# Performance work log

Measured on AMD Instinct MI355X. Metric: run time of the kernel, lower is better.

Reference implementation:

```python
import jax, jax.numpy as jnp
import numpy as np

TOP_K = 2


def setup_inputs() -> dict:
    key = jax.random.key(0)
    ks = jax.random.split(key, 6)
    B, S, H, F, E = 4, 2048, 1024, 4096, 8
    x = jax.random.normal(ks[0], (B, S, H), dtype=jnp.float32)
    gate_w = jax.random.normal(ks[1], (E, H), dtype=jnp.float32) * 0.02
    W1 = jax.random.normal(ks[2], (E, H, F), dtype=jnp.float32) * (1.0 / np.sqrt(H))
    b1 = jnp.zeros((E, F), dtype=jnp.float32)
    W2 = jax.random.normal(ks[3], (E, F, H), dtype=jnp.float32) * (1.0 / np.sqrt(F))
    b2 = jnp.zeros((E, H), dtype=jnp.float32)
    sW1 = jax.random.normal(ks[4], (H, F), dtype=jnp.float32) * (1.0 / np.sqrt(H))
    sb1 = jnp.zeros((F,), dtype=jnp.float32)
    sW2 = jax.random.normal(ks[5], (F, H), dtype=jnp.float32) * (1.0 / np.sqrt(F))
    sb2 = jnp.zeros((H,), dtype=jnp.float32)
    return {"x": x, "gate_w": gate_w, "W1": W1, "b1": b1, "W2": W2, "b2": b2,
            "sW1": sW1, "sb1": sb1, "sW2": sW2, "sb2": sb2}


def reference(x, gate_w, W1, b1, W2, b2, sW1, sb1, sW2, sb2):
    B, S, H = x.shape
    E = gate_w.shape[0]
    x_flat = x.reshape(-1, H)                                  # [T, H]
    # --- router ---
    logits = x_flat @ gate_w.T                                 # [T, E]
    probs = jax.nn.softmax(logits.astype(jnp.float32), axis=-1)
    top_w, sel = jax.lax.top_k(probs, TOP_K)                   # [T, K], [T, K]
    top_w = top_w / jnp.sum(top_w, axis=-1, keepdims=True)
    # combine weights: zero for unselected experts -> faithful to masked gather/scatter
    combine = jnp.sum(jax.nn.one_hot(sel, E, dtype=top_w.dtype) * top_w[..., None], axis=1)  # [T, E]
    combine = combine.astype(x.dtype)
    # --- experts (dense grouped GEMM; unselected tokens contribute with weight 0) ---
    h = jax.nn.gelu(jnp.einsum('th,ehf->tef', x_flat, W1) + b1[None], approximate=False)
    y = jnp.einsum('tef,efh->teh', h, W2) + b2[None]           # [T, E, H]
    out = jnp.einsum('teh,te->th', y, combine)                 # [T, H]
    # --- shared expert ---
    sh = jax.nn.gelu(x_flat @ sW1 + sb1, approximate=False)
    out = out + sh @ sW2 + sb2
    return out.reshape(B, S, H)
```

## Files before the change

kernel.cpp:

```cpp
#include <hip/hip_runtime.h>
#include <hip/hip_bf16.h>

#define T_TOKENS 8192
#define H_DIM 1024
#define F_DIM 4096
#define N_EXP 8
#define MAX_SLOTS 25600
#define MAX_TILES 200

typedef __attribute__((ext_vector_type(8))) short short8;
typedef __attribute__((ext_vector_type(4))) float floatx4;

__device__ __forceinline__ float gelu_f(float v) {
    return 0.5f * v * (1.0f + erff(v * 0.70710678118654752440f));
}

__device__ __forceinline__ void gload_lds16(const void* g, void* l) {
    __builtin_amdgcn_global_load_lds((const __attribute__((address_space(1))) void*)g,
                                     (__attribute__((address_space(3))) void*)l,
                                     16, 0, 0);
}

__global__ __launch_bounds__(256) void convert_x_kernel(const float* __restrict__ x,
                                                        unsigned long long* __restrict__ xb,
                                                        int n4) {
    int i = blockIdx.x * 256 + threadIdx.x;
    if (i >= n4) return;
    floatx4 v = ((const floatx4*)x)[i];
    union { __hip_bfloat16 h[4]; unsigned long long u; } p;
    p.h[0] = __float2bfloat16(v.x);
    p.h[1] = __float2bfloat16(v.y);
    p.h[2] = __float2bfloat16(v.z);
    p.h[3] = __float2bfloat16(v.w);
    xb[i] = p.u;
}

__global__ __launch_bounds__(256) void transpose_convert_kernel(const float* __restrict__ in,
                                                                __hip_bfloat16* __restrict__ out,
                                                                int R, int C) {
    const float* inm = in + (size_t)blockIdx.z * R * C;
    __hip_bfloat16* outm = out + (size_t)blockIdx.z * R * C;
    __shared__ float tile[32][33];
    int r0 = blockIdx.x * 32;
    int c0 = blockIdx.y * 32;
    int tx = threadIdx.x & 31, ty = threadIdx.x >> 5;
#pragma unroll
    for (int i = 0; i < 4; i++)
        tile[ty + 8 * i][tx] = inm[(size_t)(r0 + ty + 8 * i) * C + c0 + tx];
    __syncthreads();
#pragma unroll
    for (int i = 0; i < 4; i++)
        outm[(size_t)(c0 + ty + 8 * i) * R + r0 + tx] = __float2bfloat16(tile[tx][ty + 8 * i]);
}

__global__ __launch_bounds__(256) void router_kernel(const float* __restrict__ x,
                                                     const float* __restrict__ gw,
                                                     int* __restrict__ sel_e,
                                                     float* __restrict__ sel_w,
                                                     int* __restrict__ counts) {
    int wave = threadIdx.x >> 6, lane = threadIdx.x & 63;
    int t = blockIdx.x * 4 + wave;
    const float* xt = x + (size_t)t * H_DIM;
    float acc[N_EXP];
#pragma unroll
    for (int e = 0; e < N_EXP; e++) acc[e] = 0.f;
    for (int i = 0; i < H_DIM; i += 64) {
        float xv = xt[i + lane];
#pragma unroll
        for (int e = 0; e < N_EXP; e++) acc[e] += xv * gw[e * H_DIM + i + lane];
    }
#pragma unroll
    for (int e = 0; e < N_EXP; e++) {
#pragma unroll
        for (int off = 32; off > 0; off >>= 1) acc[e] += __shfl_down(acc[e], off);
    }
    if (lane == 0) {
        float m = acc[0];
#pragma unroll
        for (int e = 1; e < N_EXP; e++) m = fmaxf(m, acc[e]);
        float p[N_EXP];
#pragma unroll
        for (int e = 0; e < N_EXP; e++) p[e] = expf(acc[e] - m);
        int i1 = 0;
#pragma unroll
        for (int e = 1; e < N_EXP; e++) if (p[e] > p[i1]) i1 = e;
        int i2 = (i1 == 0) ? 1 : 0;
#pragma unroll
        for (int e = 0; e < N_EXP; e++) if (e != i1 && p[e] > p[i2]) i2 = e;
        float s = p[i1] + p[i2];
        sel_e[2 * t]     = i1;
        sel_e[2 * t + 1] = i2;
        sel_w[2 * t]     = p[i1] / s;
        sel_w[2 * t + 1] = p[i2] / s;
        atomicAdd(&counts[i1], 1);
        atomicAdd(&counts[i2], 1);
    }
}

__global__ void offsets_kernel(const int* __restrict__ counts, int* __restrict__ off) {
    if (threadIdx.x == 0 && blockIdx.x == 0) {
        int o = 0;
#pragma unroll
        for (int e = 0; e < N_EXP; e++) {
            off[e] = o;
            o += ((counts[e] + 127) >> 7) << 7;
        }
        off[8] = o;
        off[9] = o + T_TOKENS;
    }
}

__global__ __launch_bounds__(256) void scatter_kernel(const int* __restrict__ sel_e,
                                                      const float* __restrict__ sel_w,
                                                      const int* __restrict__ off,
                                                      int* __restrict__ pos,
                                                      int* __restrict__ slot_token,
                                                      float* __restrict__ slot_weight) {
    int t = blockIdx.x * 256 + threadIdx.x;
    if (t >= T_TOKENS) return;
#pragma unroll
    for (int k = 0; k < 2; k++) {
        int e = sel_e[2 * t + k];
        int p = atomicAdd(&pos[e], 1);
        int s = off[e] + p;
        slot_token[s] = t;
        slot_weight[s] = sel_w[2 * t + k];
    }
    int s = off[8] + t;
    slot_token[s] = t;
    slot_weight[s] = 1.0f;
}

__global__ __launch_bounds__(256) void gemm1_kernel(const __hip_bfloat16* __restrict__ xb,
                                                    const __hip_bfloat16* __restrict__ w1t,
                                                    const __hip_bfloat16* __restrict__ sw1t,
                                                    const float* __restrict__ b1,
                                                    const float* __restrict__ sb1,
                                                    const int* __restrict__ slot_token,
                                                    const int* __restrict__ off,
                                                    __hip_bfloat16* __restrict__ h_buf) {
    int row0 = blockIdx.x * 128;
    if (row0 >= off[9]) return;
    int f0 = blockIdx.y * 128;
    int e = 8;
#pragma unroll
    for (int i = 0; i < 8; i++)
        if (row0 >= off[i] && row0 < off[i + 1]) e = i;
    const __hip_bfloat16* Bp = (e < 8) ? (w1t + (size_t)e * F_DIM * H_DIM) : sw1t;
    const float* bias = (e < 8) ? (b1 + (size_t)e * F_DIM) : sb1;

    __shared__ __align__(16) __hip_bfloat16 As[128 * 32];
    __shared__ __align__(16) __hip_bfloat16 Bs[128 * 32];

    int tid = threadIdx.x;
    int rA = tid >> 2, cc = tid & 3;
    int tok0 = slot_token[row0 + rA];
    int tok1 = slot_token[row0 + 64 + rA];
    int t0c = tok0 >= 0 ? tok0 : 0;
    int t1c = tok1 >= 0 ? tok1 : 0;
    const __hip_bfloat16* a0 = xb + (size_t)t0c * H_DIM + cc * 8;
    const __hip_bfloat16* a1 = xb + (size_t)t1c * H_DIM + cc * 8;
    const __hip_bfloat16* b0 = Bp + (size_t)(f0 + rA) * H_DIM + cc * 8;
    const __hip_bfloat16* b1r = Bp + (size_t)(f0 + 64 + rA) * H_DIM + cc * 8;

    int lane = tid & 63, wid = tid >> 6;
    char* asb0 = (char*)As + wid * 1024;
    char* asb1 = (char*)As + 4096 + wid * 1024;
    char* bsb0 = (char*)Bs + wid * 1024;
    char* bsb1 = (char*)Bs + 4096 + wid * 1024;

    int wm = (wid >> 1) * 64, wn = (wid & 1) * 64;
    int lr = lane & 15, q = lane >> 4;

    floatx4 acc[4][4] = {};

    for (int k0 = 0; k0 < H_DIM; k0 += 32) {
        gload_lds16(a0 + k0, asb0);
        gload_lds16(a1 + k0, asb1);
        gload_lds16(b0 + k0, bsb0);
        gload_lds16(b1r + k0, bsb1);
        __syncthreads();
        short8 af[4], bfr[4];
#pragma unroll
        for (int mt = 0; mt < 4; mt++) af[mt] = *(const short8*)(&As[(wm + mt * 16 + lr) * 32 + q * 8]);
#pragma unroll
        for (int nt = 0; nt < 4; nt++) bfr[nt] = *(const short8*)(&Bs[(wn + nt * 16 + lr) * 32 + q * 8]);
#pragma unroll
        for (int mt = 0; mt < 4; mt++)
#pragma unroll
            for (int nt = 0; nt < 4; nt++)
                acc[mt][nt] = __builtin_amdgcn_mfma_f32_16x16x32_bf16(af[mt], bfr[nt], acc[mt][nt], 0, 0, 0);
        __syncthreads();
    }

#pragma unroll
    for (int mt = 0; mt < 4; mt++) {
#pragma unroll
        for (int r = 0; r < 4; r++) {
            int row = wm + mt * 16 + q * 4 + r;
            int slot = row0 + row;
            int tok = slot_token[slot];
            __hip_bfloat16* hp = h_buf + (size_t)slot * F_DIM + f0;
#pragma unroll
            for (int nt = 0; nt < 4; nt++) {
                int col = wn + nt * 16 + lr;
                float v = acc[mt][nt][r] + bias[f0 + col];
                hp[col] = __float2bfloat16(tok >= 0 ? gelu_f(v) : 0.0f);
            }
        }
    }
}

__global__ __launch_bounds__(256) void gemm2_kernel(const __hip_bfloat16* __restrict__ h_buf,
                                                    const __hip_bfloat16* __restrict__ w2t,
                                                    const __hip_bfloat16* __restrict__ sw2t,
                                                    const float* __restrict__ b2,
                                                    const float* __restrict__ sb2,
                                                    const int* __restrict__ slot_token,
                                                    const float* __restrict__ slot_weight,
                                                    const int* __restrict__ off,
                                                    float* __restrict__ out) {
    int row0 = blockIdx.y * 128;
    if (row0 >= off[9]) return;
    int h0 = blockIdx.x * 128;
    int e = 8;
#pragma unroll
    for (int i = 0; i < 8; i++)
        if (row0 >= off[i] && row0 < off[i + 1]) e = i;
    const __hip_bfloat16* Bp = (e < 8) ? (w2t + (size_t)e * H_DIM * F_DIM) : sw2t;
    const float* bias = (e < 8) ? (b2 + (size_t)e * H_DIM) : sb2;

    __shared__ __align__(16) __hip_bfloat16 As[128 * 32];
    __shared__ __align__(16) __hip_bfloat16 Bs[128 * 32];

    int tid = threadIdx.x;
    int rA = tid >> 2, cc = tid & 3;
    const __hip_bfloat16* a0 = h_buf + (size_t)(row0 + rA) * F_DIM + cc * 8;
    const __hip_bfloat16* a1 = h_buf + (size_t)(row0 + 64 + rA) * F_DIM + cc * 8;
    const __hip_bfloat16* b0 = Bp + (size_t)(h0 + rA) * F_DIM + cc * 8;
    const __hip_bfloat16* b1r = Bp + (size_t)(h0 + 64 + rA) * F_DIM + cc * 8;

    int lane = tid & 63, wid = tid >> 6;
    char* asb0 = (char*)As + wid * 1024;
    char* asb1 = (char*)As + 4096 + wid * 1024;
    char* bsb0 = (char*)Bs + wid * 1024;
    char* bsb1 = (char*)Bs + 4096 + wid * 1024;

    int wm = (wid >> 1) * 64, wn = (wid & 1) * 64;
    int lr = lane & 15, q = lane >> 4;

    floatx4 acc[4][4] = {};

    for (int k0 = 0; k0 < F_DIM; k0 += 32) {
        gload_lds16(a0 + k0, asb0);
        gload_lds16(a1 + k0, asb1);
        gload_lds16(b0 + k0, bsb0);
        gload_lds16(b1r + k0, bsb1);
        __syncthreads();
        short8 af[4], bfr[4];
#pragma unroll
        for (int mt = 0; mt < 4; mt++) af[mt] = *(const short8*)(&As[(wm + mt * 16 + lr) * 32 + q * 8]);
#pragma unroll
        for (int nt = 0; nt < 4; nt++) bfr[nt] = *(const short8*)(&Bs[(wn + nt * 16 + lr) * 32 + q * 8]);
#pragma unroll
        for (int mt = 0; mt < 4; mt++)
#pragma unroll
            for (int nt = 0; nt < 4; nt++)
                acc[mt][nt] = __builtin_amdgcn_mfma_f32_16x16x32_bf16(af[mt], bfr[nt], acc[mt][nt], 0, 0, 0);
        __syncthreads();
    }

#pragma unroll
    for (int mt = 0; mt < 4; mt++) {
#pragma unroll
        for (int r = 0; r < 4; r++) {
            int row = wm + mt * 16 + q * 4 + r;
            int slot = row0 + row;
            int tok = slot_token[slot];
            if (tok >= 0) {
                float w = slot_weight[slot];
                float* op = out + (size_t)tok * H_DIM + h0;
#pragma unroll
                for (int nt = 0; nt < 4; nt++) {
                    int col = wn + nt * 16 + lr;
                    atomicAdd(&op[col], w * (acc[mt][nt][r] + bias[h0 + col]));
                }
            }
        }
    }
}

extern "C" void kernel_launch(void* const* d_in, const int* in_sizes, int n_in,
                              void* d_out, int out_size, void* d_ws, size_t ws_size,
                              hipStream_t stream) {
    (void)in_sizes; (void)n_in; (void)ws_size;
    const float* x   = (const float*)d_in[0];
    const float* gw  = (const float*)d_in[1];
    const float* W1  = (const float*)d_in[2];
    const float* b1  = (const float*)d_in[3];
    const float* W2  = (const float*)d_in[4];
    const float* b2  = (const float*)d_in[5];
    const float* sW1 = (const float*)d_in[6];
    const float* sb1 = (const float*)d_in[7];
    const float* sW2 = (const float*)d_in[8];
    const float* sb2 = (const float*)d_in[9];
    float* out = (float*)d_out;

    char* ws = (char*)d_ws;
    size_t o = 0;
    auto alloc = [&](size_t bytes) -> void* {
        void* p = ws + o;
        o += (bytes + 255) & ~(size_t)255;
        return p;
    };
    __hip_bfloat16* xb    = (__hip_bfloat16*)alloc((size_t)T_TOKENS * H_DIM * 2);
    __hip_bfloat16* w1t   = (__hip_bfloat16*)alloc((size_t)N_EXP * H_DIM * F_DIM * 2);
    __hip_bfloat16* w2t   = (__hip_bfloat16*)alloc((size_t)N_EXP * H_DIM * F_DIM * 2);
    __hip_bfloat16* sw1t  = (__hip_bfloat16*)alloc((size_t)H_DIM * F_DIM * 2);
    __hip_bfloat16* sw2t  = (__hip_bfloat16*)alloc((size_t)H_DIM * F_DIM * 2);
    __hip_bfloat16* h_buf = (__hip_bfloat16*)alloc((size_t)MAX_SLOTS * F_DIM * 2);
    int*   slot_token  = (int*)alloc(MAX_SLOTS * 4);
    float* slot_weight = (float*)alloc(MAX_SLOTS * 4);
    int*   sel_e = (int*)alloc((size_t)T_TOKENS * 2 * 4);
    float* sel_w = (float*)alloc((size_t)T_TOKENS * 2 * 4);
    int*   ctrl  = (int*)alloc(64 * 4);
    int* counts = ctrl;
    int* pos    = ctrl + 8;
    int* off    = ctrl + 16;

    hipMemsetAsync(d_out, 0, (size_t)out_size * sizeof(float), stream);
    hipMemsetAsync(ctrl, 0, 64 * 4, stream);
    hipMemsetAsync(slot_token, 0xFF, MAX_SLOTS * 4, stream);

    int n4 = T_TOKENS * H_DIM / 4;
    convert_x_kernel<<<(n4 + 255) / 256, 256, 0, stream>>>(x, (unsigned long long*)xb, n4);

    transpose_convert_kernel<<<dim3(H_DIM / 32, F_DIM / 32, N_EXP), 256, 0, stream>>>(W1, w1t, H_DIM, F_DIM);
    transpose_convert_kernel<<<dim3(F_DIM / 32, H_DIM / 32, N_EXP), 256, 0, stream>>>(W2, w2t, F_DIM, H_DIM);
    transpose_convert_kernel<<<dim3(H_DIM / 32, F_DIM / 32, 1), 256, 0, stream>>>(sW1, sw1t, H_DIM, F_DIM);
    transpose_convert_kernel<<<dim3(F_DIM / 32, H_DIM / 32, 1), 256, 0, stream>>>(sW2, sw2t, F_DIM, H_DIM);

    router_kernel<<<T_TOKENS / 4, 256, 0, stream>>>(x, gw, sel_e, sel_w, counts);
    offsets_kernel<<<1, 64, 0, stream>>>(counts, off);
    scatter_kernel<<<T_TOKENS / 256, 256, 0, stream>>>(sel_e, sel_w, off, pos, slot_token, slot_weight);

    gemm1_kernel<<<dim3(MAX_TILES, F_DIM / 128), 256, 0, stream>>>(
        xb, w1t, sw1t, b1, sb1, slot_token, off, h_buf);
    gemm2_kernel<<<dim3(H_DIM / 128, MAX_TILES), 256, 0, stream>>>(
        h_buf, w2t, sw2t, b2, sb2, slot_token, slot_weight, off, out);
}
```

Baseline: 1.558 ms.

## Double-buffer GEMM LDS tiles, vectorize weight transpose, reorder gemm1 grid

```diff
diff --git a/kernel.cpp b/kernel.cpp
--- a/kernel.cpp
+++ b/kernel.cpp
@@ -40,17 +40,30 @@
                                                                 int R, int C) {
     const float* inm = in + (size_t)blockIdx.z * R * C;
     __hip_bfloat16* outm = out + (size_t)blockIdx.z * R * C;
-    __shared__ float tile[32][33];
-    int r0 = blockIdx.x * 32;
-    int c0 = blockIdx.y * 32;
-    int tx = threadIdx.x & 31, ty = threadIdx.x >> 5;
-#pragma unroll
-    for (int i = 0; i < 4; i++)
-        tile[ty + 8 * i][tx] = inm[(size_t)(r0 + ty + 8 * i) * C + c0 + tx];
+    __shared__ float tile[64][65];
+    int r0 = blockIdx.x * 64, c0 = blockIdx.y * 64;
+    int t = threadIdx.x;
+    int cr = t & 15;
+    int rr = t >> 4;
+#pragma unroll
+    for (int i = 0; i < 4; i++) {
+        floatx4 v = *(const floatx4*)(inm + (size_t)(r0 + rr + 16 * i) * C + c0 + cr * 4);
+        tile[rr + 16 * i][cr * 4 + 0] = v.x;
+        tile[rr + 16 * i][cr * 4 + 1] = v.y;
+        tile[rr + 16 * i][cr * 4 + 2] = v.z;
+        tile[rr + 16 * i][cr * 4 + 3] = v.w;
+    }
     __syncthreads();
-#pragma unroll
-    for (int i = 0; i < 4; i++)
-        outm[(size_t)(c0 + ty + 8 * i) * R + r0 + tx] = __float2bfloat16(tile[tx][ty + 8 * i]);
+    int cw = t >> 3;
+    int rw = (t & 7) * 8;
+#pragma unroll
+    for (int i = 0; i < 2; i++) {
+        int c = cw + 32 * i;
+        union { __hip_bfloat16 h[8]; short8 s; } p;
+#pragma unroll
+        for (int j = 0; j < 8; j++) p.h[j] = __float2bfloat16(tile[rw + j][c]);
+        *(short8*)(outm + (size_t)(c0 + c) * R + r0 + rw) = p.s;
+    }
 }
 
 __global__ __launch_bounds__(256) void router_kernel(const float* __restrict__ x,
@@ -139,9 +152,9 @@
                                                     const int* __restrict__ slot_token,
                                                     const int* __restrict__ off,
                                                     __hip_bfloat16* __restrict__ h_buf) {
-    int row0 = blockIdx.x * 128;
+    int row0 = blockIdx.y * 128;
     if (row0 >= off[9]) return;
-    int f0 = blockIdx.y * 128;
+    int f0 = blockIdx.x * 128;
     int e = 8;
 #pragma unroll
     for (int i = 0; i < 8; i++)
@@ -149,8 +162,8 @@
     const __hip_bfloat16* Bp = (e < 8) ? (w1t + (size_t)e * F_DIM * H_DIM) : sw1t;
     const float* bias = (e < 8) ? (b1 + (size_t)e * F_DIM) : sb1;
 
-    __shared__ __align__(16) __hip_bfloat16 As[128 * 32];
-    __shared__ __align__(16) __hip_bfloat16 Bs[128 * 32];
+    __shared__ __align__(16) __hip_bfloat16 As[2 * 128 * 32];
+    __shared__ __align__(16) __hip_bfloat16 Bs[2 * 128 * 32];
 
     int tid = threadIdx.x;
     int rA = tid >> 2, cc = tid & 3;
@@ -164,33 +177,42 @@
     const __hip_bfloat16* b1r = Bp + (size_t)(f0 + 64 + rA) * H_DIM + cc * 8;
 
     int lane = tid & 63, wid = tid >> 6;
-    char* asb0 = (char*)As + wid * 1024;
-    char* asb1 = (char*)As + 4096 + wid * 1024;
-    char* bsb0 = (char*)Bs + wid * 1024;
-    char* bsb1 = (char*)Bs + 4096 + wid * 1024;
+    char* asb = (char*)As + wid * 1024;
+    char* bsb = (char*)Bs + wid * 1024;
 
     int wm = (wid >> 1) * 64, wn = (wid & 1) * 64;
     int lr = lane & 15, q = lane >> 4;
 
     floatx4 acc[4][4] = {};
 
-    for (int k0 = 0; k0 < H_DIM; k0 += 32) {
-        gload_lds16(a0 + k0, asb0);
-        gload_lds16(a1 + k0, asb1);
-        gload_lds16(b0 + k0, bsb0);
-        gload_lds16(b1r + k0, bsb1);
+    gload_lds16(a0, asb);
+    gload_lds16(a1, asb + 4096);
+    gload_lds16(b0, bsb);
+    gload_lds16(b1r, bsb + 4096);
+
+    int buf = 0;
+    for (int k0 = 0; k0 < H_DIM; k0 += 32, buf ^= 1) {
         __syncthreads();
+        if (k0 + 32 < H_DIM) {
+            int kn = k0 + 32;
+            int bo = (buf ^ 1) * 8192;
+            gload_lds16(a0 + kn, asb + bo);
+            gload_lds16(a1 + kn, asb + bo + 4096);
+            gload_lds16(b0 + kn, bsb + bo);
+            gload_lds16(b1r + kn, bsb + bo + 4096);
+        }
+        const __hip_bfloat16* Ab = As + buf * 4096;
+        const __hip_bfloat16* Bb = Bs + buf * 4096;
         short8 af[4], bfr[4];
 #pragma unroll
-        for (int mt = 0; mt < 4; mt++) af[mt] = *(const short8*)(&As[(wm + mt * 16 + lr) * 32 + q * 8]);
-#pragma unroll
-        for (int nt = 0; nt < 4; nt++) bfr[nt] = *(const short8*)(&Bs[(wn + nt * 16 + lr) * 32 + q * 8]);
+        for (int mt = 0; mt < 4; mt++) af[mt] = *(const short8*)(&Ab[(wm + mt * 16 + lr) * 32 + q * 8]);
+#pragma unroll
+        for (int nt = 0; nt < 4; nt++) bfr[nt] = *(const short8*)(&Bb[(wn + nt * 16 + lr) * 32 + q * 8]);
 #pragma unroll
         for (int mt = 0; mt < 4; mt++)
 #pragma unroll
             for (int nt = 0; nt < 4; nt++)
                 acc[mt][nt] = __builtin_amdgcn_mfma_f32_16x16x32_bf16(af[mt], bfr[nt], acc[mt][nt], 0, 0, 0);
-        __syncthreads();
     }
 
 #pragma unroll
@@ -230,8 +252,8 @@
     const __hip_bfloat16* Bp = (e < 8) ? (w2t + (size_t)e * H_DIM * F_DIM) : sw2t;
     const float* bias = (e < 8) ? (b2 + (size_t)e * H_DIM) : sb2;
 
-    __shared__ __align__(16) __hip_bfloat16 As[128 * 32];
-    __shared__ __align__(16) __hip_bfloat16 Bs[128 * 32];
+    __shared__ __align__(16) __hip_bfloat16 As[2 * 128 * 32];
+    __shared__ __align__(16) __hip_bfloat16 Bs[2 * 128 * 32];
 
     int tid = threadIdx.x;
     int rA = tid >> 2, cc = tid & 3;
@@ -241,33 +263,42 @@
     const __hip_bfloat16* b1r = Bp + (size_t)(h0 + 64 + rA) * F_DIM + cc * 8;
 
     int lane = tid & 63, wid = tid >> 6;
-    char* asb0 = (char*)As + wid * 1024;
-    char* asb1 = (char*)As + 4096 + wid * 1024;
-    char* bsb0 = (char*)Bs + wid * 1024;
-    char* bsb1 = (char*)Bs + 4096 + wid * 1024;
+    char* asb = (char*)As + wid * 1024;
+    char* bsb = (char*)Bs + wid * 1024;
 
     int wm = (wid >> 1) * 64, wn = (wid & 1) * 64;
     int lr = lane & 15, q = lane >> 4;
 
     floatx4 acc[4][4] = {};
 
-    for (int k0 = 0; k0 < F_DIM; k0 += 32) {
-        gload_lds16(a0 + k0, asb0);
-        gload_lds16(a1 + k0, asb1);
-        gload_lds16(b0 + k0, bsb0);
-        gload_lds16(b1r + k0, bsb1);
+    gload_lds16(a0, asb);
+    gload_lds16(a1, asb + 4096);
+    gload_lds16(b0, bsb);
+    gload_lds16(b1r, bsb + 4096);
+
+    int buf = 0;
+    for (int k0 = 0; k0 < F_DIM; k0 += 32, buf ^= 1) {
         __syncthreads();
+        if (k0 + 32 < F_DIM) {
+            int kn = k0 + 32;
+            int bo = (buf ^ 1) * 8192;
+            gload_lds16(a0 + kn, asb + bo);
+            gload_lds16(a1 + kn, asb + bo + 4096);
+            gload_lds16(b0 + kn, bsb + bo);
+            gload_lds16(b1r + kn, bsb + bo + 4096);
+        }
+        const __hip_bfloat16* Ab = As + buf * 4096;
+        const __hip_bfloat16* Bb = Bs + buf * 4096;
         short8 af[4], bfr[4];
 #pragma unroll
-        for (int mt = 0; mt < 4; mt++) af[mt] = *(const short8*)(&As[(wm + mt * 16 + lr) * 32 + q * 8]);
-#pragma unroll
-        for (int nt = 0; nt < 4; nt++) bfr[nt] = *(const short8*)(&Bs[(wn + nt * 16 + lr) * 32 + q * 8]);
+        for (int mt = 0; mt < 4; mt++) af[mt] = *(const short8*)(&Ab[(wm + mt * 16 + lr) * 32 + q * 8]);
+#pragma unroll
+        for (int nt = 0; nt < 4; nt++) bfr[nt] = *(const short8*)(&Bb[(wn + nt * 16 + lr) * 32 + q * 8]);
 #pragma unroll
         for (int mt = 0; mt < 4; mt++)
 #pragma unroll
             for (int nt = 0; nt < 4; nt++)
                 acc[mt][nt] = __builtin_amdgcn_mfma_f32_16x16x32_bf16(af[mt], bfr[nt], acc[mt][nt], 0, 0, 0);
-        __syncthreads();
     }
 
 #pragma unroll
@@ -335,16 +366,16 @@
     int n4 = T_TOKENS * H_DIM / 4;
     convert_x_kernel<<<(n4 + 255) / 256, 256, 0, stream>>>(x, (unsigned long long*)xb, n4);
 
-    transpose_convert_kernel<<<dim3(H_DIM / 32, F_DIM / 32, N_EXP), 256, 0, stream>>>(W1, w1t, H_DIM, F_DIM);
-    transpose_convert_kernel<<<dim3(F_DIM / 32, H_DIM / 32, N_EXP), 256, 0, stream>>>(W2, w2t, F_DIM, H_DIM);
-    transpose_convert_kernel<<<dim3(H_DIM / 32, F_DIM / 32, 1), 256, 0, stream>>>(sW1, sw1t, H_DIM, F_DIM);
-    transpose_convert_kernel<<<dim3(F_DIM / 32, H_DIM / 32, 1), 256, 0, stream>>>(sW2, sw2t, F_DIM, H_DIM);
+    transpose_convert_kernel<<<dim3(H_DIM / 64, F_DIM / 64, N_EXP), 256, 0, stream>>>(W1, w1t, H_DIM, F_DIM);
+    transpose_convert_kernel<<<dim3(F_DIM / 64, H_DIM / 64, N_EXP), 256, 0, stream>>>(W2, w2t, F_DIM, H_DIM);
+    transpose_convert_kernel<<<dim3(H_DIM / 64, F_DIM / 64, 1), 256, 0, stream>>>(sW1, sw1t, H_DIM, F_DIM);
+    transpose_convert_kernel<<<dim3(F_DIM / 64, H_DIM / 64, 1), 256, 0, stream>>>(sW2, sw2t, F_DIM, H_DIM);
 
     router_kernel<<<T_TOKENS / 4, 256, 0, stream>>>(x, gw, sel_e, sel_w, counts);
     offsets_kernel<<<1, 64, 0, stream>>>(counts, off);
     scatter_kernel<<<T_TOKENS / 256, 256, 0, stream>>>(sel_e, sel_w, off, pos, slot_token, slot_weight);
 
-    gemm1_kernel<<<dim3(MAX_TILES, F_DIM / 128), 256, 0, stream>>>(
+    gemm1_kernel<<<dim3(F_DIM / 128, MAX_TILES), 256, 0, stream>>>(
         xb, w1t, sw1t, b1, sb1, slot_token, off, h_buf);
     gemm2_kernel<<<dim3(H_DIM / 128, MAX_TILES), 256, 0, stream>>>(
         h_buf, w2t, sw2t, b2, sb2, slot_token, slot_weight, off, out);
```

Result: no change. 1.561 ms (+0.2%).
